# Kernel tuning notes

Measured on AMD Instinct MI355X. Metric: run time of the kernel, lower is better.

Reference implementation:

```python
import jax, jax.numpy as jnp
import numpy as np

N = 50000      # nodes
F_IN = 128     # in_features
F_OUT = 128    # out_features
E = 800000     # edges (avg degree 16)


def setup_inputs() -> dict:
    key = jax.random.key(0)
    k = jax.random.split(key, 6)
    x = jax.random.normal(k[0], (N, F_IN), dtype=jnp.float32)
    h0 = jax.random.normal(k[1], (N, F_IN), dtype=jnp.float32)
    edge_row = jax.random.randint(k[2], (E,), 0, N, dtype=jnp.int32)
    edge_col = jax.random.randint(k[3], (E,), 0, N, dtype=jnp.int32)
    # normalized-Laplacian-like positive weights
    edge_val = jax.random.uniform(k[4], (E,), dtype=jnp.float32)
    stdv = 1.0 / np.sqrt(F_OUT)
    weight = jax.random.uniform(k[5], (F_IN, F_OUT), dtype=jnp.float32,
                                minval=-stdv, maxval=stdv)
    return {
        "input": x,
        "h0": h0,
        "edge_row": edge_row,
        "edge_col": edge_col,
        "edge_val": edge_val,
        "weight": weight,
        "lamda": jnp.float32(0.5),
        "alpha": jnp.float32(0.1),
        "l": 4,  # layer index (python int)
    }


def reference(input, h0, edge_row, edge_col, edge_val, weight, lamda, alpha, l):
    # theta = log(lamda / l + 1)
    theta = jnp.log(lamda / l + 1.0)
    # hi = spmm(G, input): gather source features, scale by edge value, scatter-add to rows
    msgs = edge_val[:, None] * input[edge_col]              # [E, F]
    hi = jax.ops.segment_sum(msgs, edge_row, num_segments=N)  # [N, F]
    # variant=False: support == r == (1-alpha)*hi + alpha*h0
    support = (1.0 - alpha) * hi + alpha * h0
    out = theta * (support @ weight) + (1.0 - theta) * support
    # residual=True
    out = out + input
    return out
```

## Files before the change

### kernel.cpp

```cpp
#include <hip/hip_runtime.h>
#include <math.h>

#define NF 128
#define SCAN_B 1024


__device__ __forceinline__ unsigned short f2bf(float f) {
    unsigned int u = __float_as_uint(f);
    u = (u + 0x7fffu + ((u >> 16) & 1u)) >> 16;
    return (unsigned short)u;
}

__global__ __launch_bounds__(256) void cvt_kernel(
    const float* __restrict__ x, uint* __restrict__ xb, int n8) {
    int i = blockIdx.x * 256 + threadIdx.x;
    if (i >= n8) return;
    float4 a = ((const float4*)x)[i * 2];
    float4 b = ((const float4*)x)[i * 2 + 1];
    uint4 o;
    o.x = (uint)f2bf(a.x) | ((uint)f2bf(a.y) << 16);
    o.y = (uint)f2bf(a.z) | ((uint)f2bf(a.w) << 16);
    o.z = (uint)f2bf(b.x) | ((uint)f2bf(b.y) << 16);
    o.w = (uint)f2bf(b.z) | ((uint)f2bf(b.w) << 16);
    ((uint4*)xb)[i] = o;
}


__global__ __launch_bounds__(256) void hist_kernel(
    const int* __restrict__ erow, int* __restrict__ cnt, int E_) {
    int e = blockIdx.x * 256 + threadIdx.x;
    if (e < E_) atomicAdd(&cnt[erow[e]], 1);
}

__global__ __launch_bounds__(SCAN_B) void scanA_kernel(
    const int* __restrict__ cnt, int* __restrict__ bsum, int N_) {
    __shared__ int buf[SCAN_B];
    int t = threadIdx.x;
    int i = blockIdx.x * SCAN_B + t;
    buf[t] = (i < N_) ? cnt[i] : 0;
    __syncthreads();
    for (int d = SCAN_B / 2; d > 0; d >>= 1) {
        if (t < d) buf[t] += buf[t + d];
        __syncthreads();
    }
    if (t == 0) bsum[blockIdx.x] = buf[0];
}

__global__ __launch_bounds__(SCAN_B) void scanC_kernel(
    const int* __restrict__ cnt, const int* __restrict__ bsum,
    int* __restrict__ off, int* __restrict__ pos, int N_, int nb) {
    __shared__ int buf[SCAN_B];
    __shared__ int bpre_sh;
    int t = threadIdx.x;
    if (t < 64) {
        int v0 = (t < nb) ? bsum[t] : 0;
        int v = v0;
        for (int d = 1; d < 64; d <<= 1) {
            int u = __shfl_up(v, d, 64);
            if (t >= d) v += u;
        }
        if (t == (int)blockIdx.x) bpre_sh = v - v0;
        if (blockIdx.x == 0 && t == nb - 1) off[N_] = v;
    }
    int i = blockIdx.x * SCAN_B + t;
    int v = (i < N_) ? cnt[i] : 0;
    buf[t] = v;
    __syncthreads();
    for (int d = 1; d < SCAN_B; d <<= 1) {
        int add = (t >= d) ? buf[t - d] : 0;
        __syncthreads();
        buf[t] += add;
        __syncthreads();
    }
    if (i < N_) {
        int o = bpre_sh + buf[t] - v;
        off[i] = o;
        pos[i] = o;
    }
}

__global__ __launch_bounds__(256) void fill_kernel(
    const int* __restrict__ erow, const int* __restrict__ ecol,
    const float* __restrict__ evalv, int* __restrict__ pos,
    int2* __restrict__ epack, int E_) {
    int e = blockIdx.x * 256 + threadIdx.x;
    if (e >= E_) return;
    int p = atomicAdd(&pos[erow[e]], 1);
    int2 pk;
    pk.x = ecol[e];
    pk.y = __float_as_int(evalv[e]);
    epack[p] = pk;
}


#define UNPK_FMA(u, v, a0, a1)                         \
    a0 += (v) * __uint_as_float((u) << 16);            \
    a1 += (v) * __uint_as_float((u) & 0xffff0000u);

__global__ __launch_bounds__(256) void spmm_kernel(
    const unsigned short* __restrict__ xb, const float* __restrict__ h0,
    const int* __restrict__ off, const int2* __restrict__ epack,
    float* __restrict__ sup, const float* __restrict__ alpha_p, int N_) {
    int w = (blockIdx.x * 256 + threadIdx.x) >> 6;
    if (w >= N_) return;
    int lane = threadIdx.x & 63;
    int g    = lane >> 4;
    int seg  = lane & 15;
    int s = off[w], e = off[w + 1];
    float acc[8] = {};
    int i = s + g;
    for (; i + 4 < e; i += 8) {
        int2 e0 = epack[i];
        int2 e1 = epack[i + 4];
        float v0 = __int_as_float(e0.y);
        float v1 = __int_as_float(e1.y);
        uint4 a = *(const uint4*)(xb + (size_t)e0.x * NF + seg * 8);
        uint4 b = *(const uint4*)(xb + (size_t)e1.x * NF + seg * 8);
        UNPK_FMA(a.x, v0, acc[0], acc[1]);
        UNPK_FMA(a.y, v0, acc[2], acc[3]);
        UNPK_FMA(a.z, v0, acc[4], acc[5]);
        UNPK_FMA(a.w, v0, acc[6], acc[7]);
        UNPK_FMA(b.x, v1, acc[0], acc[1]);
        UNPK_FMA(b.y, v1, acc[2], acc[3]);
        UNPK_FMA(b.z, v1, acc[4], acc[5]);
        UNPK_FMA(b.w, v1, acc[6], acc[7]);
    }
    if (i < e) {
        int2 e0 = epack[i];
        float v0 = __int_as_float(e0.y);
        uint4 a = *(const uint4*)(xb + (size_t)e0.x * NF + seg * 8);
        UNPK_FMA(a.x, v0, acc[0], acc[1]);
        UNPK_FMA(a.y, v0, acc[2], acc[3]);
        UNPK_FMA(a.z, v0, acc[4], acc[5]);
        UNPK_FMA(a.w, v0, acc[6], acc[7]);
    }
#pragma unroll
    for (int j = 0; j < 8; j++) {
        acc[j] += __shfl_xor(acc[j], 16, 64);
        acc[j] += __shfl_xor(acc[j], 32, 64);
    }
    if (g == 0) {
        float alpha = *alpha_p;
        float oma = 1.0f - alpha;
        const float* h = h0 + (size_t)w * NF + seg * 8;
        float4 ha = *(const float4*)h;
        float4 hb = *(const float4*)(h + 4);
        float4 o1, o2;
        o1.x = oma * acc[0] + alpha * ha.x;
        o1.y = oma * acc[1] + alpha * ha.y;
        o1.z = oma * acc[2] + alpha * ha.z;
        o1.w = oma * acc[3] + alpha * ha.w;
        o2.x = oma * acc[4] + alpha * hb.x;
        o2.y = oma * acc[5] + alpha * hb.y;
        o2.z = oma * acc[6] + alpha * hb.z;
        o2.w = oma * acc[7] + alpha * hb.w;
        float* d = sup + (size_t)w * NF + seg * 8;
        *(float4*)d = o1;
        *(float4*)(d + 4) = o2;
    }
}


__global__ __launch_bounds__(256) void gemm_epilogue_kernel(
    const float* __restrict__ sup, const float* __restrict__ W,
    const float* __restrict__ inp, float* __restrict__ out,
    const float* __restrict__ lamda_p, const int* __restrict__ l_p, int n_rows) {
    __shared__ float Ws[NF * NF];
    int tid = threadIdx.x;
    for (int i = tid; i < NF * NF / 4; i += 256)
        ((float4*)Ws)[i] = ((const float4*)W)[i];
    __syncthreads();

    float theta = logf((*lamda_p) / (float)(*l_p) + 1.0f);
    float omt = 1.0f - theta;

    int m0   = blockIdx.x * 32;
    int tcol = tid & 31;
    int trow = tid >> 5;
    int n    = tcol * 4;
    int mbase = m0 + trow * 4;

    int mr[4];
#pragma unroll
    for (int r = 0; r < 4; r++) {
        int m = mbase + r;
        mr[r] = (m < n_rows) ? m : (n_rows - 1);
    }

    float acc[4][4] = {};
    for (int k = 0; k < NF; k += 4) {
        float4 srow[4];
#pragma unroll
        for (int r = 0; r < 4; r++)
            srow[r] = *(const float4*)&sup[(size_t)mr[r] * NF + k];
#pragma unroll
        for (int kk = 0; kk < 4; kk++) {
            float4 w = *(const float4*)&Ws[(k + kk) * NF + n];
#pragma unroll
            for (int r = 0; r < 4; r++) {
                float s = (&srow[r].x)[kk];
                acc[r][0] += s * w.x;
                acc[r][1] += s * w.y;
                acc[r][2] += s * w.z;
                acc[r][3] += s * w.w;
            }
        }
    }

#pragma unroll
    for (int r = 0; r < 4; r++) {
        int m = mbase + r;
        if (m >= n_rows) break;
        float4 sv = *(const float4*)&sup[(size_t)m * NF + n];
        float4 iv = *(const float4*)&inp[(size_t)m * NF + n];
        float4 o;
        o.x = theta * acc[r][0] + omt * sv.x + iv.x;
        o.y = theta * acc[r][1] + omt * sv.y + iv.y;
        o.z = theta * acc[r][2] + omt * sv.z + iv.z;
        o.w = theta * acc[r][3] + omt * sv.w + iv.w;
        *(float4*)&out[(size_t)m * NF + n] = o;
    }
}

extern "C" void kernel_launch(void* const* d_in, const int* in_sizes, int n_in,
                              void* d_out, int out_size, void* d_ws, size_t ws_size,
                              hipStream_t stream) {
    const float* x       = (const float*)d_in[0];
    const float* h0      = (const float*)d_in[1];
    const int*   erow    = (const int*)d_in[2];
    const int*   ecol    = (const int*)d_in[3];
    const float* evalv   = (const float*)d_in[4];
    const float* W       = (const float*)d_in[5];
    const float* lamda_p = (const float*)d_in[6];
    const float* alpha_p = (const float*)d_in[7];
    const int*   l_p     = (const int*)d_in[8];

    int N_ = in_sizes[0] / NF;
    int E_ = in_sizes[2];
    int nb = (N_ + SCAN_B - 1) / SCAN_B;

    char* ws = (char*)d_ws;
    size_t o = 0;
    auto alloc = [&](size_t bytes) { char* p = ws + o; o = (o + bytes + 255) & ~(size_t)255; return p; };
    float* sup   = (float*)alloc((size_t)N_ * NF * sizeof(float));
    unsigned short* xb = (unsigned short*)alloc((size_t)N_ * NF * 2);
    int*   cnt   = (int*)  alloc((size_t)N_ * sizeof(int));
    int*   off   = (int*)  alloc((size_t)(N_ + 1) * sizeof(int));
    int*   pos   = (int*)  alloc((size_t)N_ * sizeof(int));
    int2*  epack = (int2*) alloc((size_t)E_ * sizeof(int2));
    int*   bsum  = (int*)  alloc((size_t)nb * sizeof(int));

    float* out = (float*)d_out;

    int n8 = N_ * NF / 8;
    cvt_kernel<<<(n8 + 255) / 256, 256, 0, stream>>>(x, (uint*)xb, n8);

    hipMemsetAsync(cnt, 0, (size_t)N_ * sizeof(int), stream);
    hist_kernel<<<(E_ + 255) / 256, 256, 0, stream>>>(erow, cnt, E_);
    scanA_kernel<<<nb, SCAN_B, 0, stream>>>(cnt, bsum, N_);
    scanC_kernel<<<nb, SCAN_B, 0, stream>>>(cnt, bsum, off, pos, N_, nb);
    fill_kernel<<<(E_ + 255) / 256, 256, 0, stream>>>(erow, ecol, evalv, pos, epack, E_);

    int blocks = (N_ * 64 + 255) / 256;
    spmm_kernel<<<blocks, 256, 0, stream>>>(xb, h0, off, epack, sup, alpha_p, N_);

    gemm_epilogue_kernel<<<(N_ + 31) / 32, 256, 0, stream>>>(
        sup, W, x, out, lamda_p, l_p, N_);
}
```

Baseline: 275.9 us.

## Store support in bf16 and compute dense GEMM with MFMA bf16 instructions

The SpMM kernel now writes the support matrix as bf16 instead of fp32, halving that intermediate's write and read traffic. A pre-transposed bf16 copy of W is built by a small kernel. The scalar-FMA GEMM with shared-memory W is replaced by per-wave 16x16x32 bf16 MFMA tiles. The epilogue reads bf16 support for the (1-theta) term, which lowers precision of the residual path. Epilogue stores are scalar per element, so they are less coalesced than before.

```diff
diff --git a/kernel.cpp b/kernel.cpp
--- a/kernel.cpp
+++ b/kernel.cpp
@@ -3,12 +3,18 @@
 
 #define NF 128
 #define SCAN_B 1024
+
+typedef __bf16 bf16x8 __attribute__((ext_vector_type(8)));
+typedef float  f32x4  __attribute__((ext_vector_type(4)));
 
 
 __device__ __forceinline__ unsigned short f2bf(float f) {
     unsigned int u = __float_as_uint(f);
     u = (u + 0x7fffu + ((u >> 16) & 1u)) >> 16;
     return (unsigned short)u;
+}
+__device__ __forceinline__ float bf2f(unsigned short s) {
+    return __uint_as_float((unsigned int)s << 16);
 }
 
 __global__ __launch_bounds__(256) void cvt_kernel(
@@ -23,6 +29,13 @@
     o.z = (uint)f2bf(b.x) | ((uint)f2bf(b.y) << 16);
     o.w = (uint)f2bf(b.z) | ((uint)f2bf(b.w) << 16);
     ((uint4*)xb)[i] = o;
+}
+
+__global__ __launch_bounds__(256) void cvtW_kernel(
+    const float* __restrict__ W, unsigned short* __restrict__ Wt) {
+    int idx = blockIdx.x * 256 + threadIdx.x;
+    int k = idx >> 7, n = idx & 127;
+    Wt[n * NF + k] = f2bf(W[k * NF + n]);
 }
 
 
@@ -100,7 +113,7 @@
 __global__ __launch_bounds__(256) void spmm_kernel(
     const unsigned short* __restrict__ xb, const float* __restrict__ h0,
     const int* __restrict__ off, const int2* __restrict__ epack,
-    float* __restrict__ sup, const float* __restrict__ alpha_p, int N_) {
+    unsigned short* __restrict__ supb, const float* __restrict__ alpha_p, int N_) {
     int w = (blockIdx.x * 256 + threadIdx.x) >> 6;
     if (w >= N_) return;
     int lane = threadIdx.x & 63;
@@ -145,80 +158,63 @@
         const float* h = h0 + (size_t)w * NF + seg * 8;
         float4 ha = *(const float4*)h;
         float4 hb = *(const float4*)(h + 4);
-        float4 o1, o2;
-        o1.x = oma * acc[0] + alpha * ha.x;
-        o1.y = oma * acc[1] + alpha * ha.y;
-        o1.z = oma * acc[2] + alpha * ha.z;
-        o1.w = oma * acc[3] + alpha * ha.w;
-        o2.x = oma * acc[4] + alpha * hb.x;
-        o2.y = oma * acc[5] + alpha * hb.y;
-        o2.z = oma * acc[6] + alpha * hb.z;
-        o2.w = oma * acc[7] + alpha * hb.w;
-        float* d = sup + (size_t)w * NF + seg * 8;
-        *(float4*)d = o1;
-        *(float4*)(d + 4) = o2;
-    }
-}
-
-
-__global__ __launch_bounds__(256) void gemm_epilogue_kernel(
-    const float* __restrict__ sup, const float* __restrict__ W,
-    const float* __restrict__ inp, float* __restrict__ out,
+        float o0 = oma * acc[0] + alpha * ha.x;
+        float o1 = oma * acc[1] + alpha * ha.y;
+        float o2 = oma * acc[2] + alpha * ha.z;
+        float o3 = oma * acc[3] + alpha * ha.w;
+        float o4 = oma * acc[4] + alpha * hb.x;
+        float o5 = oma * acc[5] + alpha * hb.y;
+        float o6 = oma * acc[6] + alpha * hb.z;
+        float o7 = oma * acc[7] + alpha * hb.w;
+        uint4 pk;
+        pk.x = (uint)f2bf(o0) | ((uint)f2bf(o1) << 16);
+        pk.y = (uint)f2bf(o2) | ((uint)f2bf(o3) << 16);
+        pk.z = (uint)f2bf(o4) | ((uint)f2bf(o5) << 16);
+        pk.w = (uint)f2bf(o6) | ((uint)f2bf(o7) << 16);
+        *(uint4*)(supb + (size_t)w * NF + seg * 8) = pk;
+    }
+}
+
+
+__global__ __launch_bounds__(256) void gemm_mfma_kernel(
+    const unsigned short* __restrict__ supb, const unsigned short* __restrict__ Wt,
+    const float* __restrict__ x, float* __restrict__ out,
     const float* __restrict__ lamda_p, const int* __restrict__ l_p, int n_rows) {
-    __shared__ float Ws[NF * NF];
-    int tid = threadIdx.x;
-    for (int i = tid; i < NF * NF / 4; i += 256)
-        ((float4*)Ws)[i] = ((const float4*)W)[i];
-    __syncthreads();
+    int wave = threadIdx.x >> 6;
+    int lane = threadIdx.x & 63;
+    int m0 = blockIdx.x * 64 + wave * 16;
+    if (m0 >= n_rows) return;
 
     float theta = logf((*lamda_p) / (float)(*l_p) + 1.0f);
     float omt = 1.0f - theta;
 
-    int m0   = blockIdx.x * 32;
-    int tcol = tid & 31;
-    int trow = tid >> 5;
-    int n    = tcol * 4;
-    int mbase = m0 + trow * 4;
-
-    int mr[4];
-#pragma unroll
-    for (int r = 0; r < 4; r++) {
-        int m = mbase + r;
-        mr[r] = (m < n_rows) ? m : (n_rows - 1);
-    }
-
-    float acc[4][4] = {};
-    for (int k = 0; k < NF; k += 4) {
-        float4 srow[4];
-#pragma unroll
-        for (int r = 0; r < 4; r++)
-            srow[r] = *(const float4*)&sup[(size_t)mr[r] * NF + k];
-#pragma unroll
-        for (int kk = 0; kk < 4; kk++) {
-            float4 w = *(const float4*)&Ws[(k + kk) * NF + n];
-#pragma unroll
-            for (int r = 0; r < 4; r++) {
-                float s = (&srow[r].x)[kk];
-                acc[r][0] += s * w.x;
-                acc[r][1] += s * w.y;
-                acc[r][2] += s * w.z;
-                acc[r][3] += s * w.w;
-            }
+    int lr = lane & 15;
+    int kg = lane >> 4;
+
+    bf16x8 afr[4];
+    const unsigned short* abase = supb + (size_t)(m0 + lr) * NF + kg * 8;
+#pragma unroll
+    for (int kt = 0; kt < 4; kt++)
+        afr[kt] = *reinterpret_cast<const bf16x8*>(abase + kt * 32);
+
+#pragma unroll
+    for (int nt = 0; nt < 8; nt++) {
+        int n0 = nt * 16;
+        const unsigned short* bbase = Wt + (size_t)(n0 + lr) * NF + kg * 8;
+        f32x4 acc = {0.f, 0.f, 0.f, 0.f};
+#pragma unroll
+        for (int kt = 0; kt < 4; kt++) {
+            bf16x8 bfr = *reinterpret_cast<const bf16x8*>(bbase + kt * 32);
+            acc = __builtin_amdgcn_mfma_f32_16x16x32_bf16(afr[kt], bfr, acc, 0, 0, 0);
         }
-    }
-
-#pragma unroll
-    for (int r = 0; r < 4; r++) {
-        int m = mbase + r;
-        if (m >= n_rows) break;
-        float4 sv = *(const float4*)&sup[(size_t)m * NF + n];
-        float4 iv = *(const float4*)&inp[(size_t)m * NF + n];
-        float4 o;
-        o.x = theta * acc[r][0] + omt * sv.x + iv.x;
-        o.y = theta * acc[r][1] + omt * sv.y + iv.y;
-        o.z = theta * acc[r][2] + omt * sv.z + iv.z;
-        o.w = theta * acc[r][3] + omt * sv.w + iv.w;
-        *(float4*)&out[(size_t)m * NF + n] = o;
+        int ncol = n0 + lr;
+#pragma unroll
+        for (int j = 0; j < 4; j++) {
+            int m = m0 + kg * 4 + j;
+            float sv = bf2f(supb[(size_t)m * NF + ncol]);
+            float xv = x[(size_t)m * NF + ncol];
+            out[(size_t)m * NF + ncol] = theta * acc[j] + omt * sv + xv;
+        }
     }
 }
 
@@ -242,8 +238,9 @@
     char* ws = (char*)d_ws;
     size_t o = 0;
     auto alloc = [&](size_t bytes) { char* p = ws + o; o = (o + bytes + 255) & ~(size_t)255; return p; };
-    float* sup   = (float*)alloc((size_t)N_ * NF * sizeof(float));
-    unsigned short* xb = (unsigned short*)alloc((size_t)N_ * NF * 2);
+    unsigned short* supb = (unsigned short*)alloc((size_t)N_ * NF * 2);
+    unsigned short* xb   = (unsigned short*)alloc((size_t)N_ * NF * 2);
+    unsigned short* Wt   = (unsigned short*)alloc((size_t)NF * NF * 2);
     int*   cnt   = (int*)  alloc((size_t)N_ * sizeof(int));
     int*   off   = (int*)  alloc((size_t)(N_ + 1) * sizeof(int));
     int*   pos   = (int*)  alloc((size_t)N_ * sizeof(int));
@@ -254,6 +251,7 @@
 
     int n8 = N_ * NF / 8;
     cvt_kernel<<<(n8 + 255) / 256, 256, 0, stream>>>(x, (uint*)xb, n8);
+    cvtW_kernel<<<NF * NF / 256, 256, 0, stream>>>(W, Wt);
 
     hipMemsetAsync(cnt, 0, (size_t)N_ * sizeof(int), stream);
     hist_kernel<<<(E_ + 255) / 256, 256, 0, stream>>>(erow, cnt, E_);
@@ -262,8 +260,8 @@
     fill_kernel<<<(E_ + 255) / 256, 256, 0, stream>>>(erow, ecol, evalv, pos, epack, E_);
 
     int blocks = (N_ * 64 + 255) / 256;
-    spmm_kernel<<<blocks, 256, 0, stream>>>(xb, h0, off, epack, sup, alpha_p, N_);
-
-    gemm_epilogue_kernel<<<(N_ + 31) / 32, 256, 0, stream>>>(
-        sup, W, x, out, lamda_p, l_p, N_);
-}
+    spmm_kernel<<<blocks, 256, 0, stream>>>(xb, h0, off, epack, supb, alpha_p, N_);
+
+    gemm_mfma_kernel<<<(N_ + 63) / 64, 256, 0, stream>>>(
+        supb, Wt, x, out, lamda_p, l_p, N_);
+}
```

Result: faster. 261.0 us (-5.4%).
